# Optimization experiments

Measured on AMD Instinct MI355X. Metric: run time of the kernel, lower is better.

Reference implementation:

```python
import jax, jax.numpy as jnp
import numpy as np

L = 32        # label_num = len(label2idx)
SOS = 0       # label2idx['[SOS]']
END = 1       # label2idx['[END]']
NEG = -10000.0
B, T = 512, 1024


def setup_inputs() -> dict:
    key = jax.random.key(0)
    k1, k2, k3 = jax.random.split(key, 3)
    emission = jax.random.normal(k1, (B, T, L), dtype=jnp.float32)
    label_ids = jax.random.randint(k2, (B, T), 0, L)
    transitions = jax.random.normal(k3, (L, L), dtype=jnp.float32)
    # CrfLayer.__init__: forbid transitions into [SOS] and out of [END]
    transitions = transitions.at[SOS, :].set(NEG).at[:, END].set(NEG)
    return {"emission": emission, "label_ids": label_ids, "transitions": transitions}


def reference(emission, label_ids, transitions):
    b, t, l = emission.shape
    # ---- _forward_alg: log-partition via sequential logsumexp recurrence ----
    alpha0 = jnp.full((b, l), NEG, dtype=emission.dtype).at[:, SOS].set(0.0)
    feats_t = jnp.transpose(emission, (1, 0, 2))  # [T, B, L]

    def step(alpha, feat):
        # aa[b, j, i] = alpha[b, i] + feat[b, j] + transitions[j, i]
        aa = alpha[:, None, :] + feat[:, :, None] + transitions[None, :, :]
        return jax.nn.logsumexp(aa, axis=2), None

    alpha, _ = jax.lax.scan(step, alpha0, feats_t)
    forward_score = jax.nn.logsumexp(alpha + transitions[END][None, :], axis=1)  # [B]

    # ---- _score_sentence: score of the gold path ----
    tags = jnp.concatenate(
        [jnp.full((b, 1), SOS, dtype=label_ids.dtype), label_ids], axis=1)  # [B, T+1]
    trans_score = transitions[tags[:, 1:], tags[:, :-1]].sum(axis=1)          # [B]
    emit_score = jnp.take_along_axis(
        emission, tags[:, 1:, None].astype(jnp.int32), axis=2)[..., 0].sum(axis=1)  # [B]
    gold_score = trans_score + emit_score + transitions[END, tags[:, -1]]

    # loss = sum(forward_score - gold_score)
    return jnp.sum(forward_score - gold_score)
```

## Files before the change

### kernel.cpp

```cpp
#include <hip/hip_runtime.h>


typedef float  f32x16 __attribute__((ext_vector_type(16)));
typedef short  s16x8  __attribute__((ext_vector_type(8)));
typedef float  f32x2  __attribute__((ext_vector_type(2)));

#define TT 1024
#define LL 32
#define BB 512
#define NC 8
#define CL 128
#define MS 33

union Frag { s16x8 v; unsigned u[4]; };

__device__ __forceinline__ unsigned pack_bf16(float lo, float hi) {
    return __builtin_amdgcn_perm(__float_as_uint(hi), __float_as_uint(lo), 0x07060302u);
}

__device__ __forceinline__ void skew_sleep_q(int phase) {
    int p = phase & 3;
    if (p == 1) __builtin_amdgcn_s_sleep(5);
    else if (p == 2) __builtin_amdgcn_s_sleep(10);
    else if (p == 3) __builtin_amdgcn_s_sleep(15);
}

__global__ __launch_bounds__(NC * 64, 4) void crf_fused_kernel(
    const float* __restrict__ emission,
    const int*   __restrict__ label_ids,
    const float* __restrict__ transitions,
    float*       __restrict__ out)
{
    __shared__ __align__(16) float shM[NC][32 * MS];
    __shared__ float shQ[2][64];
    __shared__ float tgArr[NC];
    __shared__ int   capArr[NC];

    const int tid  = threadIdx.x;
    const int w    = tid >> 6;
    const int lane = tid & 63;
    const int j    = lane & 31;
    const int h    = lane >> 5;
    const int b    = blockIdx.x;
    const int t0   = w * CL;

    const int*   labB = label_ids + b * TT + t0;
    const float* emB  = emission + ((size_t)b * TT + t0) * LL + j;

    {
        float g = 0.0f;
#pragma unroll
        for (int u = 0; u < 2; ++u) {
            int tt = t0 + 64 * u + lane;
            int l1 = labB[64 * u + lane];
            int l0 = (tt == 0) ? 0 : label_ids[b * TT + tt - 1];
            g += transitions[(l1 << 5) + l0];
            g += emission[((size_t)b * TT + tt) * LL + l1];
            if (tt == TT - 1) g += transitions[32 + l1];
        }
#pragma unroll
        for (int m = 32; m >= 1; m >>= 1) g += __shfl_xor(g, m, 64);
        if (lane == 0) tgArr[w] = g;
    }

    const float* trow = transitions + j * 32;
    f32x2 E0v[4], E1v[4];
#pragma unroll
    for (int p = 0; p < 4; ++p) {
        int c0 = ((2 * p) & 3)     + 8 * ((2 * p) >> 2)     + 4 * h;
        int c1 = ((2 * p + 1) & 3) + 8 * ((2 * p + 1) >> 2) + 4 * h;
        E0v[p][0] = __expf(trow[c0]);      E0v[p][1] = __expf(trow[c1]);
        E1v[p][0] = __expf(trow[16 + c0]); E1v[p][1] = __expf(trow[16 + c1]);
    }

    Frag B0, B1;
#pragma unroll
    for (int i = 0; i < 8; ++i) {
        int row = (i & 3) + 8 * (i >> 2) + 4 * h;
        B0.v[i] = (short)((row == j)      ? 0x3F80 : 0);
        B1.v[i] = (short)((row + 16 == j) ? 0x3F80 : 0);
    }

    f32x16 zc, acc;
#pragma unroll
    for (int i = 0; i < 16; ++i) zc[i] = 0.0f;

    float ring[8];
#pragma unroll
    for (int s = 0; s < 8; ++s) ring[s] = emB[s * LL];

    float sc = 1.0f;
    int   Cap = 0, elast = 0;

    skew_sleep_q((w >> 2) + ((blockIdx.x & 1) << 1));

    auto step = [&](int k, int s, bool refill) {
        float feat = ring[k];
        float fs = ((k & 3) == 0) ? (__expf(feat) * sc) : __expf(feat);
        f32x2 fs2; fs2[0] = fs; fs2[1] = fs;

        Frag A0, A1;
#pragma unroll
        for (int p = 0; p < 4; ++p) {
            f32x2 a = fs2 * E0v[p];
            f32x2 c = fs2 * E1v[p];
            A0.u[p] = pack_bf16(a[0], a[1]);
            A1.u[p] = pack_bf16(c[0], c[1]);
        }

        acc = __builtin_amdgcn_mfma_f32_32x32x16_bf16(A0.v, B0.v, zc, 0, 0, 0);
        acc = __builtin_amdgcn_mfma_f32_32x32x16_bf16(A1.v, B1.v, acc, 0, 0, 0);

        if ((k & 3) == 3) {
            int pb = __builtin_amdgcn_readlane(__float_as_int(acc[2]), 0);
            int e  = ((pb >> 23) & 0xff) - 127;
            sc = __int_as_float((127 - e) << 23);
            Cap += e;
            elast = e;
        }

        if (refill) ring[k] = emB[(s + 8) * LL];

#pragma unroll
        for (int p = 0; p < 4; ++p) {
            B0.u[p] = pack_bf16(acc[2 * p],     acc[2 * p + 1]);
            B1.u[p] = pack_bf16(acc[8 + 2 * p], acc[9 + 2 * p]);
        }
    };

    for (int s0 = 0; s0 < CL - 8; s0 += 8) {
#pragma unroll
        for (int k = 0; k < 8; ++k) step(k, s0 + k, true);
    }
#pragma unroll
    for (int k = 0; k < 8; ++k) step(k, CL - 8 + k, false);

    Cap -= elast;

#pragma unroll
    for (int r = 0; r < 16; ++r) {
        int row = (r & 3) + 8 * (r >> 2) + 4 * h;
        shM[w][row * MS + j] = acc[r];
    }
    if (lane == 0) capArr[w] = Cap;

    __syncthreads();

    if (w == 0) {
        const float Eend = __expf(transitions[32 + j]);
        float q = (j == 0) ? 1.0f : 0.0f;
        int   Cq = 0;
        float gold = 0.0f;

#pragma unroll
        for (int c = 0; c < NC; ++c) {
            shQ[c & 1][lane] = q;
            asm volatile("s_waitcnt lgkmcnt(0)" ::: "memory");
            __builtin_amdgcn_wave_barrier();
            const float* Mrow = &shM[c][j * MS];
            const float* qv   = &shQ[c & 1][h * 32];
            float a0 = 0.f, a1 = 0.f, a2 = 0.f, a3 = 0.f;
#pragma unroll
            for (int i = 0; i < 32; i += 4) {
                a0 = fmaf(Mrow[i],     qv[i],     a0);
                a1 = fmaf(Mrow[i + 1], qv[i + 1], a1);
                a2 = fmaf(Mrow[i + 2], qv[i + 2], a2);
                a3 = fmaf(Mrow[i + 3], qv[i + 3], a3);
            }
            float qn = (a0 + a1) + (a2 + a3);
            int pb = __builtin_amdgcn_readlane(__float_as_int(qn), 2);
            int e  = ((pb >> 23) & 0xff) - 127;
            qn *= __int_as_float((127 - e) << 23);
            Cq += e + capArr[c];
            gold += tgArr[c];
            q = qn;
        }

        float v = q * Eend;
#pragma unroll
        for (int m = 16; m >= 1; m >>= 1) v += __shfl_xor(v, m, 32);
        float fwd = __logf(v) + (float)Cq * 0.69314718055994531f;

        if (lane == 0) atomicAdd(out, fwd - gold);
    }
}

extern "C" void kernel_launch(void* const* d_in, const int* in_sizes, int n_in,
                              void* d_out, int out_size, void* d_ws, size_t ws_size,
                              hipStream_t stream)
{
    const float* emission    = (const float*)d_in[0];
    const int*   label_ids   = (const int*)d_in[1];
    const float* transitions = (const float*)d_in[2];
    float* out = (float*)d_out;

    (void)hipMemsetAsync(out, 0, sizeof(float), stream);
    crf_fused_kernel<<<BB, NC * 64, 0, stream>>>(emission, label_ids, transitions, out);
}
```

Baseline: 134.6 us.

## Pair consecutive CRF steps into one precomputed two-step transfer matrix

Restructures the chunked CRF recurrence so that each iteration first builds a two-step transfer matrix (diag(f1)·E^T·diag(f2)·E) with MFMA, off the critical chain, then applies it to the running state. The serial MFMA dependency chain is halved, and the next step's exp-emissions are staged through shared memory. It also removes the skewed s_sleep start and lowers the launch-bounds occupancy hint from 4 to 3 to make room for more registers. The cost is extra MFMA and packing work per pair and an additional bf16 rounding of the intermediate product.

```diff
diff --git a/kernel.cpp b/kernel.cpp
--- a/kernel.cpp
+++ b/kernel.cpp
@@ -4,6 +4,7 @@
 typedef float  f32x16 __attribute__((ext_vector_type(16)));
 typedef short  s16x8  __attribute__((ext_vector_type(8)));
 typedef float  f32x2  __attribute__((ext_vector_type(2)));
+typedef float  f32x4  __attribute__((ext_vector_type(4)));
 
 #define TT 1024
 #define LL 32
@@ -18,20 +19,14 @@
     return __builtin_amdgcn_perm(__float_as_uint(hi), __float_as_uint(lo), 0x07060302u);
 }
 
-__device__ __forceinline__ void skew_sleep_q(int phase) {
-    int p = phase & 3;
-    if (p == 1) __builtin_amdgcn_s_sleep(5);
-    else if (p == 2) __builtin_amdgcn_s_sleep(10);
-    else if (p == 3) __builtin_amdgcn_s_sleep(15);
-}
-
-__global__ __launch_bounds__(NC * 64, 4) void crf_fused_kernel(
+__global__ __launch_bounds__(NC * 64, 3) void crf_fused_kernel(
     const float* __restrict__ emission,
     const int*   __restrict__ label_ids,
     const float* __restrict__ transitions,
     float*       __restrict__ out)
 {
     __shared__ __align__(16) float shM[NC][32 * MS];
+    __shared__ __align__(16) float shF[NC][2][32];
     __shared__ float shQ[2][64];
     __shared__ float tgArr[NC];
     __shared__ int   capArr[NC];
@@ -65,20 +60,25 @@
 
     const float* trow = transitions + j * 32;
     f32x2 E0v[4], E1v[4];
+    f32x2 EcA[4], EcB[4];
 #pragma unroll
     for (int p = 0; p < 4; ++p) {
         int c0 = ((2 * p) & 3)     + 8 * ((2 * p) >> 2)     + 4 * h;
         int c1 = ((2 * p + 1) & 3) + 8 * ((2 * p + 1) >> 2) + 4 * h;
         E0v[p][0] = __expf(trow[c0]);      E0v[p][1] = __expf(trow[c1]);
         E1v[p][0] = __expf(trow[16 + c0]); E1v[p][1] = __expf(trow[16 + c1]);
-    }
-
-    Frag B0, B1;
+        EcA[p][0] = __expf(transitions[c0 * 32 + j]);
+        EcA[p][1] = __expf(transitions[c1 * 32 + j]);
+        EcB[p][0] = __expf(transitions[(c0 + 16) * 32 + j]);
+        EcB[p][1] = __expf(transitions[(c1 + 16) * 32 + j]);
+    }
+
+    Frag Bf0, Bf1;
 #pragma unroll
     for (int i = 0; i < 8; ++i) {
         int row = (i & 3) + 8 * (i >> 2) + 4 * h;
-        B0.v[i] = (short)((row == j)      ? 0x3F80 : 0);
-        B1.v[i] = (short)((row + 16 == j) ? 0x3F80 : 0);
+        Bf0.v[i] = (short)((row == j)      ? 0x3F80 : 0);
+        Bf1.v[i] = (short)((row + 16 == j) ? 0x3F80 : 0);
     }
 
     f32x16 zc, acc;
@@ -88,30 +88,61 @@
     float ring[8];
 #pragma unroll
     for (int s = 0; s < 8; ++s) ring[s] = emB[s * LL];
+
+    shF[w][0][j] = __expf(ring[0]);
 
     float sc = 1.0f;
     int   Cap = 0, elast = 0;
 
-    skew_sleep_q((w >> 2) + ((blockIdx.x & 1) << 1));
-
-    auto step = [&](int k, int s, bool refill) {
-        float feat = ring[k];
-        float fs = ((k & 3) == 0) ? (__expf(feat) * sc) : __expf(feat);
-        f32x2 fs2; fs2[0] = fs; fs2[1] = fs;
-
-        Frag A0, A1;
-#pragma unroll
-        for (int p = 0; p < 4; ++p) {
-            f32x2 a = fs2 * E0v[p];
-            f32x2 c = fs2 * E1v[p];
-            A0.u[p] = pack_bf16(a[0], a[1]);
-            A1.u[p] = pack_bf16(c[0], c[1]);
-        }
-
-        acc = __builtin_amdgcn_mfma_f32_32x32x16_bf16(A0.v, B0.v, zc, 0, 0, 0);
-        acc = __builtin_amdgcn_mfma_f32_32x32x16_bf16(A1.v, B1.v, acc, 0, 0, 0);
-
-        if ((k & 3) == 3) {
+    auto pairstep = [&](int k1, int k2, int s, bool refill, int pk) {
+        float f2 = __expf(ring[k2]);
+        if (pk == 0) f2 *= sc;
+        f32x2 f2v; f2v[0] = f2; f2v[1] = f2;
+        Frag V20, V21;
+#pragma unroll
+        for (int q = 0; q < 4; ++q) {
+            f32x2 a = f2v * E0v[q];
+            f32x2 c = f2v * E1v[q];
+            V20.u[q] = pack_bf16(a[0], a[1]);
+            V21.u[q] = pack_bf16(c[0], c[1]);
+        }
+
+        const f32x4* fp = (const f32x4*)(&shF[w][pk][0]);
+        f32x4 fA = fp[h], fB = fp[2 + h], fC = fp[4 + h], fD = fp[6 + h];
+        Frag T0, T1;
+        {
+            f32x2 u;
+            u[0] = fA[0]; u[1] = fA[1]; u *= EcA[0]; T0.u[0] = pack_bf16(u[0], u[1]);
+            u[0] = fA[2]; u[1] = fA[3]; u *= EcA[1]; T0.u[1] = pack_bf16(u[0], u[1]);
+            u[0] = fB[0]; u[1] = fB[1]; u *= EcA[2]; T0.u[2] = pack_bf16(u[0], u[1]);
+            u[0] = fB[2]; u[1] = fB[3]; u *= EcA[3]; T0.u[3] = pack_bf16(u[0], u[1]);
+            u[0] = fC[0]; u[1] = fC[1]; u *= EcB[0]; T1.u[0] = pack_bf16(u[0], u[1]);
+            u[0] = fC[2]; u[1] = fC[3]; u *= EcB[1]; T1.u[1] = pack_bf16(u[0], u[1]);
+            u[0] = fD[0]; u[1] = fD[1]; u *= EcB[2]; T1.u[2] = pack_bf16(u[0], u[1]);
+            u[0] = fD[2]; u[1] = fD[3]; u *= EcB[3]; T1.u[3] = pack_bf16(u[0], u[1]);
+        }
+
+        f32x16 pacc = __builtin_amdgcn_mfma_f32_32x32x16_bf16(T0.v, V20.v, zc, 0, 0, 0);
+        pacc = __builtin_amdgcn_mfma_f32_32x32x16_bf16(T1.v, V21.v, pacc, 0, 0, 0);
+
+        shF[w][pk ^ 1][j] = __expf(ring[(k1 + 2) & 7]);
+
+        if (refill) {
+            ring[k1] = emB[(s + 8) * LL];
+            ring[k2] = emB[(s + 9) * LL];
+        }
+
+        Frag PF0, PF1;
+#pragma unroll
+        for (int q = 0; q < 4; ++q) {
+            PF0.u[q] = pack_bf16(pacc[2 * q],     pacc[2 * q + 1]);
+            PF1.u[q] = pack_bf16(pacc[8 + 2 * q], pacc[9 + 2 * q]);
+        }
+
+        acc = __builtin_amdgcn_mfma_f32_32x32x16_bf16(PF0.v, Bf0.v, zc, 0, 0, 0);
+        acc = __builtin_amdgcn_mfma_f32_32x32x16_bf16(PF1.v, Bf1.v, acc, 0, 0, 0);
+
+        if (pk) {
             int pb = __builtin_amdgcn_readlane(__float_as_int(acc[2]), 0);
             int e  = ((pb >> 23) & 0xff) - 127;
             sc = __int_as_float((127 - e) << 23);
@@ -119,21 +150,23 @@
             elast = e;
         }
 
-        if (refill) ring[k] = emB[(s + 8) * LL];
-
-#pragma unroll
-        for (int p = 0; p < 4; ++p) {
-            B0.u[p] = pack_bf16(acc[2 * p],     acc[2 * p + 1]);
-            B1.u[p] = pack_bf16(acc[8 + 2 * p], acc[9 + 2 * p]);
+#pragma unroll
+        for (int q = 0; q < 4; ++q) {
+            Bf0.u[q] = pack_bf16(acc[2 * q],     acc[2 * q + 1]);
+            Bf1.u[q] = pack_bf16(acc[8 + 2 * q], acc[9 + 2 * q]);
         }
     };
 
     for (int s0 = 0; s0 < CL - 8; s0 += 8) {
-#pragma unroll
-        for (int k = 0; k < 8; ++k) step(k, s0 + k, true);
-    }
-#pragma unroll
-    for (int k = 0; k < 8; ++k) step(k, CL - 8 + k, false);
+        pairstep(0, 1, s0 + 0, true, 0);
+        pairstep(2, 3, s0 + 2, true, 1);
+        pairstep(4, 5, s0 + 4, true, 0);
+        pairstep(6, 7, s0 + 6, true, 1);
+    }
+    pairstep(0, 1, CL - 8, false, 0);
+    pairstep(2, 3, CL - 6, false, 1);
+    pairstep(4, 5, CL - 4, false, 0);
+    pairstep(6, 7, CL - 2, false, 1);
 
     Cap -= elast;
 
```

Measured after the change: 144.5 us. 1.07x slower.

## Move emission scaling from MFMA A operand to accumulator rows via LDS

Applied to the files above, without the earlier changes.

Keeps exp(transitions) as a constant bf16 A fragment and applies the per-step emission factor after the MFMA, multiplying accumulator rows by exp(feat) read from a double-buffered LDS array. Each step's next exp(feat) is written to LDS by the owning lane, and the accumulator fragment layout reads it back as vectors. This removes the per-step A-fragment rebuild (multiplies and packs) but adds LDS traffic and read-after-write ordering within the wave, whose correctness depends on wave-synchronous execution without explicit waits. The staggered s_sleep skew at kernel start is also removed.

```diff
diff --git a/kernel.cpp b/kernel.cpp
--- a/kernel.cpp
+++ b/kernel.cpp
@@ -4,6 +4,7 @@
 typedef float  f32x16 __attribute__((ext_vector_type(16)));
 typedef short  s16x8  __attribute__((ext_vector_type(8)));
 typedef float  f32x2  __attribute__((ext_vector_type(2)));
+typedef float  f32x4  __attribute__((ext_vector_type(4)));
 
 #define TT 1024
 #define LL 32
@@ -16,13 +17,6 @@
 
 __device__ __forceinline__ unsigned pack_bf16(float lo, float hi) {
     return __builtin_amdgcn_perm(__float_as_uint(hi), __float_as_uint(lo), 0x07060302u);
-}
-
-__device__ __forceinline__ void skew_sleep_q(int phase) {
-    int p = phase & 3;
-    if (p == 1) __builtin_amdgcn_s_sleep(5);
-    else if (p == 2) __builtin_amdgcn_s_sleep(10);
-    else if (p == 3) __builtin_amdgcn_s_sleep(15);
 }
 
 __global__ __launch_bounds__(NC * 64, 4) void crf_fused_kernel(
@@ -32,6 +26,7 @@
     float*       __restrict__ out)
 {
     __shared__ __align__(16) float shM[NC][32 * MS];
+    __shared__ __align__(16) float shF[NC][2][32];
     __shared__ float shQ[2][64];
     __shared__ float tgArr[NC];
     __shared__ int   capArr[NC];
@@ -64,13 +59,13 @@
     }
 
     const float* trow = transitions + j * 32;
-    f32x2 E0v[4], E1v[4];
+    Frag Ea0, Ea1;
 #pragma unroll
     for (int p = 0; p < 4; ++p) {
         int c0 = ((2 * p) & 3)     + 8 * ((2 * p) >> 2)     + 4 * h;
         int c1 = ((2 * p + 1) & 3) + 8 * ((2 * p + 1) >> 2) + 4 * h;
-        E0v[p][0] = __expf(trow[c0]);      E0v[p][1] = __expf(trow[c1]);
-        E1v[p][0] = __expf(trow[16 + c0]); E1v[p][1] = __expf(trow[16 + c1]);
+        Ea0.u[p] = pack_bf16(__expf(trow[c0]),      __expf(trow[c1]));
+        Ea1.u[p] = pack_bf16(__expf(trow[16 + c0]), __expf(trow[16 + c1]));
     }
 
     Frag B0, B1;
@@ -89,29 +84,20 @@
 #pragma unroll
     for (int s = 0; s < 8; ++s) ring[s] = emB[s * LL];
 
+    shF[w][0][j] = __expf(ring[0]);
+
     float sc = 1.0f;
     int   Cap = 0, elast = 0;
-
-    skew_sleep_q((w >> 2) + ((blockIdx.x & 1) << 1));
+    f32x2 sm0[4], sm1[4];
 
     auto step = [&](int k, int s, bool refill) {
-        float feat = ring[k];
-        float fs = ((k & 3) == 0) ? (__expf(feat) * sc) : __expf(feat);
-        f32x2 fs2; fs2[0] = fs; fs2[1] = fs;
-
-        Frag A0, A1;
-#pragma unroll
-        for (int p = 0; p < 4; ++p) {
-            f32x2 a = fs2 * E0v[p];
-            f32x2 c = fs2 * E1v[p];
-            A0.u[p] = pack_bf16(a[0], a[1]);
-            A1.u[p] = pack_bf16(c[0], c[1]);
-        }
-
-        acc = __builtin_amdgcn_mfma_f32_32x32x16_bf16(A0.v, B0.v, zc, 0, 0, 0);
-        acc = __builtin_amdgcn_mfma_f32_32x32x16_bf16(A1.v, B1.v, acc, 0, 0, 0);
-
-        if ((k & 3) == 3) {
+        const f32x4* fp = (const f32x4*)(&shF[w][s & 1][0]);
+        f32x4 fA = fp[h], fB = fp[2 + h], fC = fp[4 + h], fD = fp[6 + h];
+
+        acc = __builtin_amdgcn_mfma_f32_32x32x16_bf16(Ea0.v, B0.v, zc, 0, 0, 0);
+        acc = __builtin_amdgcn_mfma_f32_32x32x16_bf16(Ea1.v, B1.v, acc, 0, 0, 0);
+
+        if ((s & 3) == 3) {
             int pb = __builtin_amdgcn_readlane(__float_as_int(acc[2]), 0);
             int e  = ((pb >> 23) & 0xff) - 127;
             sc = __int_as_float((127 - e) << 23);
@@ -119,12 +105,28 @@
             elast = e;
         }
 
+        {
+            float fn = __expf(ring[(k + 1) & 7]);
+            if (((s + 1) & 3) == 0) fn *= sc;
+            shF[w][(s + 1) & 1][j] = fn;
+        }
+
         if (refill) ring[k] = emB[(s + 8) * LL];
 
-#pragma unroll
-        for (int p = 0; p < 4; ++p) {
-            B0.u[p] = pack_bf16(acc[2 * p],     acc[2 * p + 1]);
-            B1.u[p] = pack_bf16(acc[8 + 2 * p], acc[9 + 2 * p]);
+        f32x2 fv, av;
+        fv[0] = fA[0]; fv[1] = fA[1]; av[0] = acc[0];  av[1] = acc[1];  sm0[0] = fv * av;
+        fv[0] = fA[2]; fv[1] = fA[3]; av[0] = acc[2];  av[1] = acc[3];  sm0[1] = fv * av;
+        fv[0] = fB[0]; fv[1] = fB[1]; av[0] = acc[4];  av[1] = acc[5];  sm0[2] = fv * av;
+        fv[0] = fB[2]; fv[1] = fB[3]; av[0] = acc[6];  av[1] = acc[7];  sm0[3] = fv * av;
+        fv[0] = fC[0]; fv[1] = fC[1]; av[0] = acc[8];  av[1] = acc[9];  sm1[0] = fv * av;
+        fv[0] = fC[2]; fv[1] = fC[3]; av[0] = acc[10]; av[1] = acc[11]; sm1[1] = fv * av;
+        fv[0] = fD[0]; fv[1] = fD[1]; av[0] = acc[12]; av[1] = acc[13]; sm1[2] = fv * av;
+        fv[0] = fD[2]; fv[1] = fD[3]; av[0] = acc[14]; av[1] = acc[15]; sm1[3] = fv * av;
+
+#pragma unroll
+        for (int q = 0; q < 4; ++q) {
+            B0.u[q] = pack_bf16(sm0[q][0], sm0[q][1]);
+            B1.u[q] = pack_bf16(sm1[q][0], sm1[q][1]);
         }
     };
 
@@ -140,7 +142,8 @@
 #pragma unroll
     for (int r = 0; r < 16; ++r) {
         int row = (r & 3) + 8 * (r >> 2) + 4 * h;
-        shM[w][row * MS + j] = acc[r];
+        float val = (r < 8) ? sm0[r >> 1][r & 1] : sm1[(r >> 1) - 4][r & 1];
+        shM[w][row * MS + j] = val;
     }
     if (lane == 0) capArr[w] = Cap;
 
```

New measurement: 134.7 us. No clear change (+0.1%).
